# Kernel optimization log

Hardware: AMD Instinct MI355X
Metric: run time of the kernel (lower is better)

Reference implementation:

```python
import jax, jax.numpy as jnp
import numpy as np

B, D, N, K = 16, 128, 16384, 64


def setup_inputs() -> dict:
    key = jax.random.key(0)
    k1, k2, k3, k4 = jax.random.split(key, 4)
    x = jax.random.normal(k1, (B, D, N), dtype=jnp.float32)
    mu = jax.random.normal(k2, (K, D), dtype=jnp.float32)
    log_sigma = 0.1 * jax.random.normal(k3, (K, D), dtype=jnp.float32)
    log_alpha = 0.1 * jax.random.normal(k4, (K,), dtype=jnp.float32)
    return {"x": x, "mu": mu, "log_sigma": log_sigma, "log_alpha": log_alpha}


def reference(x, mu, log_sigma, log_alpha):
    # x: (B, D, N) -> (B, N, D)
    xt = jnp.transpose(x, (0, 2, 1))
    # F.normalize(mu): L2-normalize each cluster center along D (eps=1e-12)
    mu_n = mu / jnp.maximum(jnp.linalg.norm(mu, axis=1, keepdims=True), 1e-12)
    sigma_inv = jnp.exp(-log_sigma)                     # (K, D)
    log_sigma_sum = jnp.sum(log_sigma, axis=1)          # (K,)
    # dist_{bnk} = sum_d (x-mu)^2 * sinv, decomposed into GEMMs
    xsq_term = jnp.einsum('bnd,kd->bnk', xt * xt, sigma_inv)
    cross = jnp.einsum('bnd,kd->bnk', xt, mu_n * sigma_inv)
    mu_term = jnp.sum(mu_n * mu_n * sigma_inv, axis=1)  # (K,)
    dist = xsq_term - 2.0 * cross + mu_term
    logits = -dist + log_alpha - 0.5 * log_sigma_sum    # (B, N, K)
    posterior = jax.nn.softmax(logits, axis=-1)
    return jnp.transpose(posterior, (0, 2, 1))          # (B, K, N)
```

## Files before the change

kernel.cpp:

```cpp
#include <hip/hip_runtime.h>

#define LOG2E 1.4426950408889634f

constexpr int Dn = 128;
constexpr int Nn = 16384;
constexpr int Kn = 64;
constexpr int Bn = 16;

typedef float f32x4 __attribute__((ext_vector_type(4)));
typedef unsigned int u32x4 __attribute__((ext_vector_type(4)));

__device__ __forceinline__ unsigned int rnhi(float f) {
    unsigned int u = __float_as_uint(f);
    return (u + 0x7FFFu + ((u >> 16) & 1u)) & 0xFFFF0000u;
}

__global__ __launch_bounds__(64) void gmm_prep(const float* __restrict__ mu,
                                               const float* __restrict__ log_sigma,
                                               const float* __restrict__ log_alpha,
                                               unsigned short* __restrict__ wfrag,
                                               float* __restrict__ cout) {
    const int k = blockIdx.x;
    const int l = threadIdx.x;
    const int d0 = 2 * l;
    float m0 = mu[k * Dn + d0];
    float m1 = mu[k * Dn + d0 + 1];
    float s0 = log_sigma[k * Dn + d0];
    float s1 = log_sigma[k * Dn + d0 + 1];
    float nrm2 = m0 * m0 + m1 * m1;
    float lss = s0 + s1;
    #pragma unroll
    for (int off = 32; off > 0; off >>= 1) {
        nrm2 += __shfl_xor(nrm2, off);
        lss  += __shfl_xor(lss, off);
    }
    const float inv_nrm = 1.0f / fmaxf(sqrtf(nrm2), 1e-12f);
    const float mn0 = m0 * inv_nrm, mn1 = m1 * inv_nrm;
    const float si0 = expf(-s0), si1 = expf(-s1);
    float mt = mn0 * mn0 * si0 + mn1 * mn1 * si1;
    #pragma unroll
    for (int off = 32; off > 0; off >>= 1) mt += __shfl_xor(mt, off);

    const float av[2] = {-si0 * LOG2E, -si1 * LOG2E};
    const float bv[2] = {2.0f * mn0 * si0 * LOG2E, 2.0f * mn1 * si1 * LOG2E};
    const int ks = k >> 4;
    #pragma unroll
    for (int dd = 0; dd < 2; ++dd) {
        const int d = d0 + dd;
        const unsigned int ah = rnhi(av[dd]);
        const unsigned int al = rnhi(av[dd] - __uint_as_float(ah));
        const unsigned int bh = rnhi(bv[dd]);
        const unsigned int bl = rnhi(bv[dd] - __uint_as_float(bh));
        const int s = d >> 5, h = (d >> 3) & 3, j = d & 7;
        const int lane = (h << 4) | (k & 15);
        const size_t base = ((size_t)((ks * 4 + s) * 4) * 64 + lane) * 8 + j;
        wfrag[base + 0 * 64 * 8] = (unsigned short)(ah >> 16);
        wfrag[base + 1 * 64 * 8] = (unsigned short)(al >> 16);
        wfrag[base + 2 * 64 * 8] = (unsigned short)(bh >> 16);
        wfrag[base + 3 * 64 * 8] = (unsigned short)(bl >> 16);
    }
    if (l == 0) cout[k] = (log_alpha[k] - 0.5f * lss - mt) * LOG2E;
}

__global__ __launch_bounds__(512)
__attribute__((amdgpu_waves_per_eu(4, 4)))
void gmm_main(const float* __restrict__ x,
              const unsigned short* __restrict__ wf,
              const float* __restrict__ cks,
              float* __restrict__ out) {
    __shared__ unsigned short sB[4][4][4][64][8];
    __shared__ float sRedM[4][64];
    __shared__ float sRedS[4][64];

    const int tid = threadIdx.x;
    const int l = tid & 63;
    const int b = blockIdx.y;
    const int nwin = blockIdx.x * 64;
    const float* xwin = x + (size_t)b * Dn * Nn + nwin;

    float xv[2][8];
    #pragma unroll
    for (int i = 0; i < 2; ++i) {
        const int o = (tid >> 6) + 8 * i;
        #pragma unroll
        for (int jj = 0; jj < 8; ++jj)
            xv[i][jj] = xwin[(size_t)(o * 8 + jj) * Nn + l];
    }
    #pragma unroll
    for (int i = 0; i < 2; ++i) {
        const int o = (tid >> 6) + 8 * i;
        const int s = o >> 2, h = o & 3;
        const int lane = (h << 4) | (l & 15), tt = l >> 4;
        unsigned int XH[4], XL[4], TH[4], TL[4];
        #pragma unroll
        for (int p = 0; p < 4; ++p) {
            const float x0 = xv[i][2 * p], x1 = xv[i][2 * p + 1];
            const float t0 = x0 * x0, t1 = x1 * x1;
            const unsigned int xh0 = rnhi(x0), xh1 = rnhi(x1);
            const unsigned int xq0 = rnhi(x0 - __uint_as_float(xh0));
            const unsigned int xq1 = rnhi(x1 - __uint_as_float(xh1));
            const unsigned int th0 = rnhi(t0), th1 = rnhi(t1);
            const unsigned int tq0 = rnhi(t0 - __uint_as_float(th0));
            const unsigned int tq1 = rnhi(t1 - __uint_as_float(th1));
            XH[p] = (xh0 >> 16) | xh1;
            XL[p] = (xq0 >> 16) | xq1;
            TH[p] = (th0 >> 16) | th1;
            TL[p] = (tq0 >> 16) | tq1;
        }
        *(u32x4*)&sB[0][s][tt][lane][0] = u32x4{XH[0], XH[1], XH[2], XH[3]};
        *(u32x4*)&sB[1][s][tt][lane][0] = u32x4{XL[0], XL[1], XL[2], XL[3]};
        *(u32x4*)&sB[2][s][tt][lane][0] = u32x4{TH[0], TH[1], TH[2], TH[3]};
        *(u32x4*)&sB[3][s][tt][lane][0] = u32x4{TL[0], TL[1], TL[2], TL[3]};
    }

    const int wid = __builtin_amdgcn_readfirstlane(tid >> 6);
    const int ks = wid & 3, tp = wid >> 2;
    u32x4 W[4][4];
    #pragma unroll
    for (int s = 0; s < 4; ++s)
        #pragma unroll
        for (int m = 0; m < 4; ++m)
            W[s][m] = *(const u32x4*)(wf + ((size_t)((ks * 4 + s) * 4 + m) * 64 + l) * 8);

    f32x4 acc[2];
    #pragma unroll
    for (int tt = 0; tt < 2; ++tt)
        #pragma unroll
        for (int r = 0; r < 4; ++r)
            acc[tt][r] = cks[ks * 16 + (l >> 4) * 4 + r];

    __syncthreads();

#define MFMA(C, A, B_) asm("v_mfma_f32_16x16x32_bf16 %0, %1, %2, %0" \
                           : "+v"(C) : "v"(A), "v"(B_))
    asm volatile("s_nop 1");
    #pragma unroll
    for (int s = 0; s < 4; ++s) {
        #pragma unroll
        for (int tt = 0; tt < 2; ++tt) {
            const int ttg = tp * 2 + tt;
            const u32x4 Xh = *(const u32x4*)&sB[0][s][ttg][l][0];
            const u32x4 Xl = *(const u32x4*)&sB[1][s][ttg][l][0];
            const u32x4 Th = *(const u32x4*)&sB[2][s][ttg][l][0];
            const u32x4 Tl = *(const u32x4*)&sB[3][s][ttg][l][0];
            MFMA(acc[tt], W[s][0], Th);
            MFMA(acc[tt], W[s][1], Th);
            MFMA(acc[tt], W[s][0], Tl);
            MFMA(acc[tt], W[s][2], Xh);
            MFMA(acc[tt], W[s][3], Xh);
            MFMA(acc[tt], W[s][2], Xl);
        }
    }
#undef MFMA
    asm volatile("s_nop 7\n\ts_nop 7");

    float mw[2];
    #pragma unroll
    for (int tt = 0; tt < 2; ++tt) {
        float m = fmaxf(fmaxf(acc[tt][0], acc[tt][1]),
                        fmaxf(acc[tt][2], acc[tt][3]));
        m = fmaxf(m, __shfl_xor(m, 16));
        m = fmaxf(m, __shfl_xor(m, 32));
        mw[tt] = m;
        if (l < 16) sRedM[ks][(tp * 2 + tt) * 16 + l] = m;
    }
    __syncthreads();
    float M[2], stot[2];
    #pragma unroll
    for (int tt = 0; tt < 2; ++tt) {
        const int ttg = tp * 2 + tt;
        float m = sRedM[0][ttg * 16 + (l & 15)];
        m = fmaxf(m, sRedM[1][ttg * 16 + (l & 15)]);
        m = fmaxf(m, sRedM[2][ttg * 16 + (l & 15)]);
        m = fmaxf(m, sRedM[3][ttg * 16 + (l & 15)]);
        M[tt] = m;
        float ssum = 0.f;
        #pragma unroll
        for (int r = 0; r < 4; ++r) {
            acc[tt][r] = __builtin_amdgcn_exp2f(acc[tt][r] - m);
            ssum += acc[tt][r];
        }
        ssum += __shfl_xor(ssum, 16);
        ssum += __shfl_xor(ssum, 32);
        if (l < 16) sRedS[ks][ttg * 16 + l] = ssum;
    }
    __syncthreads();
    #pragma unroll
    for (int tt = 0; tt < 2; ++tt) {
        const int ttg = tp * 2 + tt;
        stot[tt] = sRedS[0][ttg * 16 + (l & 15)] + sRedS[1][ttg * 16 + (l & 15)] +
                   sRedS[2][ttg * 16 + (l & 15)] + sRedS[3][ttg * 16 + (l & 15)];
    }

    #pragma unroll
    for (int tt = 0; tt < 2; ++tt) {
        const int ttg = tp * 2 + tt;
        const float inv = 1.0f / stot[tt];
        float* op = out + ((size_t)(b * Kn + ks * 16 + (l >> 4) * 4)) * Nn +
                    nwin + ttg * 16 + (l & 15);
        #pragma unroll
        for (int r = 0; r < 4; ++r) {
            *op = acc[tt][r] * inv;
            op += Nn;
        }
    }
}

extern "C" void kernel_launch(void* const* d_in, const int* in_sizes, int n_in,
                              void* d_out, int out_size, void* d_ws, size_t ws_size,
                              hipStream_t stream) {
    const float* x  = (const float*)d_in[0];
    const float* mu = (const float*)d_in[1];
    const float* ls = (const float*)d_in[2];
    const float* la = (const float*)d_in[3];
    float* out = (float*)d_out;

    unsigned short* wbuf = (unsigned short*)d_ws;
    float* cbuf = (float*)((char*)d_ws + 65536);

    gmm_prep<<<dim3(Kn), dim3(64), 0, stream>>>(mu, ls, la, wbuf, cbuf);
    gmm_main<<<dim3(Nn / 64, Bn), dim3(512), 0, stream>>>(x, wbuf, cbuf, out);
}
```

Before: 221.9 us.

## Load x straight into MFMA fragments, drop LDS staging, double tokens per block

Each wave now loads its own x values from global memory directly in MFMA B-fragment order and splits them into bf16 hi/lo inside registers. This removes the LDS staging buffer and its barrier. Each block now covers 128 tokens instead of 64, so weight fragments are reused across four tiles per wave, and the inline-asm MFMAs become compiler builtins. In exchange, each x element is loaded redundantly by the four k-slice waves (relying on cache), and the per-tile global loads are strided across rows.

```diff
diff --git a/kernel.cpp b/kernel.cpp
--- a/kernel.cpp
+++ b/kernel.cpp
@@ -1,4 +1,5 @@
 #include <hip/hip_runtime.h>
+#include <hip/hip_bf16.h>
 
 #define LOG2E 1.4426950408889634f
 
@@ -9,6 +10,7 @@
 
 typedef float f32x4 __attribute__((ext_vector_type(4)));
 typedef unsigned int u32x4 __attribute__((ext_vector_type(4)));
+typedef short short8 __attribute__((ext_vector_type(8)));
 
 __device__ __forceinline__ unsigned int rnhi(float f) {
     unsigned int u = __float_as_uint(f);
@@ -62,118 +64,104 @@
     if (l == 0) cout[k] = (log_alpha[k] - 0.5f * lss - mt) * LOG2E;
 }
 
+__device__ __forceinline__ unsigned int pk2(float a, float b) {
+    __hip_bfloat162 h = __float22bfloat162_rn(make_float2(a, b));
+    unsigned int u;
+    __builtin_memcpy(&u, &h, 4);
+    return u;
+}
+
 __global__ __launch_bounds__(512)
 __attribute__((amdgpu_waves_per_eu(4, 4)))
 void gmm_main(const float* __restrict__ x,
               const unsigned short* __restrict__ wf,
               const float* __restrict__ cks,
               float* __restrict__ out) {
-    __shared__ unsigned short sB[4][4][4][64][8];
-    __shared__ float sRedM[4][64];
-    __shared__ float sRedS[4][64];
+    __shared__ float sRedM[4][128];
+    __shared__ float sRedS[4][128];
 
     const int tid = threadIdx.x;
     const int l = tid & 63;
+    const int wid = __builtin_amdgcn_readfirstlane(tid >> 6);
+    const int ks = wid & 3;
+    const int tp = wid >> 2;
+    const int h = l >> 4;
     const int b = blockIdx.y;
-    const int nwin = blockIdx.x * 64;
+    const int nwin = blockIdx.x * 128;
     const float* xwin = x + (size_t)b * Dn * Nn + nwin;
 
-    float xv[2][8];
-    #pragma unroll
-    for (int i = 0; i < 2; ++i) {
-        const int o = (tid >> 6) + 8 * i;
-        #pragma unroll
-        for (int jj = 0; jj < 8; ++jj)
-            xv[i][jj] = xwin[(size_t)(o * 8 + jj) * Nn + l];
-    }
-    #pragma unroll
-    for (int i = 0; i < 2; ++i) {
-        const int o = (tid >> 6) + 8 * i;
-        const int s = o >> 2, h = o & 3;
-        const int lane = (h << 4) | (l & 15), tt = l >> 4;
-        unsigned int XH[4], XL[4], TH[4], TL[4];
-        #pragma unroll
-        for (int p = 0; p < 4; ++p) {
-            const float x0 = xv[i][2 * p], x1 = xv[i][2 * p + 1];
-            const float t0 = x0 * x0, t1 = x1 * x1;
-            const unsigned int xh0 = rnhi(x0), xh1 = rnhi(x1);
-            const unsigned int xq0 = rnhi(x0 - __uint_as_float(xh0));
-            const unsigned int xq1 = rnhi(x1 - __uint_as_float(xh1));
-            const unsigned int th0 = rnhi(t0), th1 = rnhi(t1);
-            const unsigned int tq0 = rnhi(t0 - __uint_as_float(th0));
-            const unsigned int tq1 = rnhi(t1 - __uint_as_float(th1));
-            XH[p] = (xh0 >> 16) | xh1;
-            XL[p] = (xq0 >> 16) | xq1;
-            TH[p] = (th0 >> 16) | th1;
-            TL[p] = (tq0 >> 16) | tq1;
+    f32x4 acc[4];
+    #pragma unroll
+    for (int tt = 0; tt < 4; ++tt)
+        #pragma unroll
+        for (int r = 0; r < 4; ++r)
+            acc[tt][r] = cks[ks * 16 + h * 4 + r];
+
+#define BC(v) __builtin_bit_cast(short8, v)
+    #pragma unroll
+    for (int s = 0; s < 4; ++s) {
+        u32x4 Ws[4];
+        #pragma unroll
+        for (int m = 0; m < 4; ++m)
+            Ws[m] = *(const u32x4*)(wf +
+                     ((size_t)((ks * 4 + s) * 4 + m) * 64 + l) * 8);
+
+        #pragma unroll
+        for (int tt = 0; tt < 4; ++tt) {
+            const int ttg = tp * 4 + tt;
+            const float* xtok = xwin + ttg * 16 + (l & 15);
+            float xv[8];
+            #pragma unroll
+            for (int j = 0; j < 8; ++j)
+                xv[j] = xtok[(size_t)(s * 32 + 8 * h + j) * Nn];
+
+            u32x4 Xh, Xl, Th, Tl;
+            #pragma unroll
+            for (int p = 0; p < 4; ++p) {
+                const float x0 = xv[2 * p], x1 = xv[2 * p + 1];
+                const float t0 = x0 * x0, t1 = x1 * x1;
+                const unsigned int xh = pk2(x0, x1);
+                Xh[p] = xh;
+                Xl[p] = pk2(x0 - __uint_as_float(xh << 16),
+                            x1 - __uint_as_float(xh & 0xFFFF0000u));
+                const unsigned int th = pk2(t0, t1);
+                Th[p] = th;
+                Tl[p] = pk2(t0 - __uint_as_float(th << 16),
+                            t1 - __uint_as_float(th & 0xFFFF0000u));
+            }
+            acc[tt] = __builtin_amdgcn_mfma_f32_16x16x32_bf16(
+                          BC(Ws[0]), BC(Th), acc[tt], 0, 0, 0);
+            acc[tt] = __builtin_amdgcn_mfma_f32_16x16x32_bf16(
+                          BC(Ws[1]), BC(Th), acc[tt], 0, 0, 0);
+            acc[tt] = __builtin_amdgcn_mfma_f32_16x16x32_bf16(
+                          BC(Ws[0]), BC(Tl), acc[tt], 0, 0, 0);
+            acc[tt] = __builtin_amdgcn_mfma_f32_16x16x32_bf16(
+                          BC(Ws[2]), BC(Xh), acc[tt], 0, 0, 0);
+            acc[tt] = __builtin_amdgcn_mfma_f32_16x16x32_bf16(
+                          BC(Ws[3]), BC(Xh), acc[tt], 0, 0, 0);
+            acc[tt] = __builtin_amdgcn_mfma_f32_16x16x32_bf16(
+                          BC(Ws[2]), BC(Xl), acc[tt], 0, 0, 0);
         }
-        *(u32x4*)&sB[0][s][tt][lane][0] = u32x4{XH[0], XH[1], XH[2], XH[3]};
-        *(u32x4*)&sB[1][s][tt][lane][0] = u32x4{XL[0], XL[1], XL[2], XL[3]};
-        *(u32x4*)&sB[2][s][tt][lane][0] = u32x4{TH[0], TH[1], TH[2], TH[3]};
-        *(u32x4*)&sB[3][s][tt][lane][0] = u32x4{TL[0], TL[1], TL[2], TL[3]};
-    }
-
-    const int wid = __builtin_amdgcn_readfirstlane(tid >> 6);
-    const int ks = wid & 3, tp = wid >> 2;
-    u32x4 W[4][4];
-    #pragma unroll
-    for (int s = 0; s < 4; ++s)
-        #pragma unroll
-        for (int m = 0; m < 4; ++m)
-            W[s][m] = *(const u32x4*)(wf + ((size_t)((ks * 4 + s) * 4 + m) * 64 + l) * 8);
-
-    f32x4 acc[2];
-    #pragma unroll
-    for (int tt = 0; tt < 2; ++tt)
-        #pragma unroll
-        for (int r = 0; r < 4; ++r)
-            acc[tt][r] = cks[ks * 16 + (l >> 4) * 4 + r];
-
-    __syncthreads();
-
-#define MFMA(C, A, B_) asm("v_mfma_f32_16x16x32_bf16 %0, %1, %2, %0" \
-                           : "+v"(C) : "v"(A), "v"(B_))
-    asm volatile("s_nop 1");
-    #pragma unroll
-    for (int s = 0; s < 4; ++s) {
-        #pragma unroll
-        for (int tt = 0; tt < 2; ++tt) {
-            const int ttg = tp * 2 + tt;
-            const u32x4 Xh = *(const u32x4*)&sB[0][s][ttg][l][0];
-            const u32x4 Xl = *(const u32x4*)&sB[1][s][ttg][l][0];
-            const u32x4 Th = *(const u32x4*)&sB[2][s][ttg][l][0];
-            const u32x4 Tl = *(const u32x4*)&sB[3][s][ttg][l][0];
-            MFMA(acc[tt], W[s][0], Th);
-            MFMA(acc[tt], W[s][1], Th);
-            MFMA(acc[tt], W[s][0], Tl);
-            MFMA(acc[tt], W[s][2], Xh);
-            MFMA(acc[tt], W[s][3], Xh);
-            MFMA(acc[tt], W[s][2], Xl);
-        }
-    }
-#undef MFMA
-    asm volatile("s_nop 7\n\ts_nop 7");
-
-    float mw[2];
-    #pragma unroll
-    for (int tt = 0; tt < 2; ++tt) {
+    }
+#undef BC
+
+    #pragma unroll
+    for (int tt = 0; tt < 4; ++tt) {
         float m = fmaxf(fmaxf(acc[tt][0], acc[tt][1]),
                         fmaxf(acc[tt][2], acc[tt][3]));
         m = fmaxf(m, __shfl_xor(m, 16));
         m = fmaxf(m, __shfl_xor(m, 32));
-        mw[tt] = m;
-        if (l < 16) sRedM[ks][(tp * 2 + tt) * 16 + l] = m;
+        if (l < 16) sRedM[ks][(tp * 4 + tt) * 16 + l] = m;
     }
     __syncthreads();
-    float M[2], stot[2];
-    #pragma unroll
-    for (int tt = 0; tt < 2; ++tt) {
-        const int ttg = tp * 2 + tt;
+    float stot[4];
+    #pragma unroll
+    for (int tt = 0; tt < 4; ++tt) {
+        const int ttg = tp * 4 + tt;
         float m = sRedM[0][ttg * 16 + (l & 15)];
         m = fmaxf(m, sRedM[1][ttg * 16 + (l & 15)]);
         m = fmaxf(m, sRedM[2][ttg * 16 + (l & 15)]);
         m = fmaxf(m, sRedM[3][ttg * 16 + (l & 15)]);
-        M[tt] = m;
         float ssum = 0.f;
         #pragma unroll
         for (int r = 0; r < 4; ++r) {
@@ -186,17 +174,17 @@
     }
     __syncthreads();
     #pragma unroll
-    for (int tt = 0; tt < 2; ++tt) {
-        const int ttg = tp * 2 + tt;
+    for (int tt = 0; tt < 4; ++tt) {
+        const int ttg = tp * 4 + tt;
         stot[tt] = sRedS[0][ttg * 16 + (l & 15)] + sRedS[1][ttg * 16 + (l & 15)] +
                    sRedS[2][ttg * 16 + (l & 15)] + sRedS[3][ttg * 16 + (l & 15)];
     }
 
     #pragma unroll
-    for (int tt = 0; tt < 2; ++tt) {
-        const int ttg = tp * 2 + tt;
+    for (int tt = 0; tt < 4; ++tt) {
+        const int ttg = tp * 4 + tt;
         const float inv = 1.0f / stot[tt];
-        float* op = out + ((size_t)(b * Kn + ks * 16 + (l >> 4) * 4)) * Nn +
+        float* op = out + ((size_t)(b * Kn + ks * 16 + h * 4)) * Nn +
                     nwin + ttg * 16 + (l & 15);
         #pragma unroll
         for (int r = 0; r < 4; ++r) {
@@ -219,5 +207,5 @@
     float* cbuf = (float*)((char*)d_ws + 65536);
 
     gmm_prep<<<dim3(Kn), dim3(64), 0, stream>>>(mu, ls, la, wbuf, cbuf);
-    gmm_main<<<dim3(Nn / 64, Bn), dim3(512), 0, stream>>>(x, wbuf, cbuf, out);
-}
+    gmm_main<<<dim3(Nn / 128, Bn), dim3(512), 0, stream>>>(x, wbuf, cbuf, out);
+}
```

Measured after the change: 239.0 us. +7.7%, slower.
